# Performance work log

Hardware: AMD Instinct MI355X
Metric: run time of the kernel (lower is better)

Reference implementation:

```python
import jax, jax.numpy as jnp
import numpy as np

N, CM, CZ, COPM = 256, 384, 128, 32
HS, DHS = 8, 48   # row-attention heads / head dim (HS*DHS == CM)
HT, DHT = 4, 32   # triangle-attention heads / head dim


def _param_shapes():
    d = {'opm_ln': (2, CM), 'opm_lr_w': (2, CM, COPM), 'opm_lr_b': (2, COPM),
         'opm_out_w': (COPM, COPM, CZ), 'opm_out_b': (CZ,),
         'ra_ln': (2, CM), 'ra_pair_ln': (2, CZ), 'ra_feat_w': (CZ, HS),
         'ra_qkv_w': (3, CM, HS, DHS), 'ra_gate_w': (CM, HS, DHS), 'ra_gate_b': (HS, DHS),
         'ra_o_w': (HS, DHS, CM), 'ra_o_b': (CM,),
         'st_ln': (2, CM), 'st_w1': (CM, 4 * CM), 'st_b1': (4 * CM,), 'st_w2': (4 * CM, CM), 'st_b2': (CM,)}
    for p in ('tmo', 'tmi'):
        d.update({p + '_ln': (2, CZ), p + '_lr_w': (2, CZ, CZ), p + '_lr_b': (2, CZ),
                  p + '_gate_w': (2, CZ, CZ), p + '_gate_b': (2, CZ), p + '_cln': (2, CZ),
                  p + '_out_w': (CZ, CZ), p + '_out_b': (CZ,), p + '_og_w': (CZ, CZ), p + '_og_b': (CZ,)})
    for p in ('tas', 'tae'):
        d.update({p + '_ln': (2, CZ), p + '_feat_w': (CZ, HT), p + '_qkv_w': (3, CZ, HT, DHT),
                  p + '_gate_w': (CZ, HT, DHT), p + '_gate_b': (HT, DHT),
                  p + '_o_w': (HT, DHT, CZ), p + '_o_b': (CZ,)})
    d.update({'pt_ln': (2, CZ), 'pt_w1': (CZ, 4 * CZ), 'pt_b1': (4 * CZ,),
              'pt_w2': (4 * CZ, CZ), 'pt_b2': (CZ,)})
    return d

_PNAMES = list(_param_shapes().keys())


def setup_inputs():
    keys = iter(jax.random.split(jax.random.key(0), 64))
    inp = {'single_act': jax.random.normal(next(keys), (1, N, CM), jnp.float32),
           'pair_act': jax.random.normal(next(keys), (N, N, CZ), jnp.float32),
           'single_mask': jnp.ones((1, N), jnp.float32),
           'pair_mask': jnp.ones((N, N), jnp.float32)}
    for name, shp in _param_shapes().items():
        p = 0.1 * jax.random.normal(next(keys), shp, jnp.float32)
        if name.endswith('_ln') or name.endswith('_cln'):
            p = p.at[0].add(1.0)  # LayerNorm scale centered at 1
        inp[name] = p
    return inp


def _ln(x, p, eps=1e-5):
    mu = jnp.mean(x, -1, keepdims=True)
    var = jnp.var(x, -1, keepdims=True)
    return (x - mu) * jax.lax.rsqrt(var + eps) * p[0] + p[1]


def _attn(q_data, m_data, bias, nb, qkv_w, gw, gb, ow, ob):
    # AlphaFold gated attention with nonbatched pair bias.
    dh = qkv_w.shape[-1]
    q = jnp.einsum('bqa,ahc->bqhc', q_data, qkv_w[0]) * (dh ** -0.5)
    k = jnp.einsum('bka,ahc->bkhc', m_data, qkv_w[1])
    v = jnp.einsum('bka,ahc->bkhc', m_data, qkv_w[2])
    logits = jnp.einsum('bqhc,bkhc->bhqk', q, k) + bias + nb[None]
    w = jax.nn.softmax(logits, axis=-1)
    wa = jnp.einsum('bhqk,bkhc->bqhc', w, v)
    wa = wa * jax.nn.sigmoid(jnp.einsum('bqc,chv->bqhv', q_data, gw) + gb)
    return jnp.einsum('bqhc,hco->bqo', wa, ow) + ob


def _opm(single, mask1, ln_p, lr_w, lr_b, out_w, out_b):
    # Outer-stack(product)-mean: single [S=1,N,CM] -> pair update [N,N,CZ]
    x = _ln(single, ln_p)
    m = mask1[..., None]
    left = m * (x @ lr_w[0] + lr_b[0])    # [1,N,COPM]
    right = m * (x @ lr_w[1] + lr_b[1])
    act = jnp.einsum('abc,ade->dceb', left, right)          # [N,COPM,COPM,N]
    act = jnp.einsum('dceb,cef->dbf', act, out_w) + out_b   # [N,N,CZ]
    norm = jnp.einsum('abc,adc->bdc', m, m)                 # [N,N,1]
    return act / (1e-3 + norm)


def _tri_mult(pair, mask2, ln_p, lr_w, lr_b, gw, gb, cln, out_w, out_b, og_w, og_b, outgoing):
    m = mask2[..., None]
    x = _ln(pair, ln_p)
    left = m * (x @ lr_w[0] + lr_b[0]) * jax.nn.sigmoid(x @ gw[0] + gb[0])
    right = m * (x @ lr_w[1] + lr_b[1]) * jax.nn.sigmoid(x @ gw[1] + gb[1])
    eq = 'ikc,jkc->ijc' if outgoing else 'kjc,kic->ijc'
    out = jnp.einsum(eq, left, right)
    out = _ln(out, cln) @ out_w + out_b
    out = out * jax.nn.sigmoid(x @ og_w + og_b)
    return pair + out


def _tri_attn(pair, mask2, ln_p, feat_w, qkv_w, gw, gb, ow, ob, per_column):
    pa = jnp.swapaxes(pair, 0, 1) if per_column else pair
    mk = jnp.swapaxes(mask2, 0, 1) if per_column else mask2
    x = _ln(pa, ln_p)
    bias = (1e9 * (mk - 1.0))[:, None, None, :]
    nb = jnp.einsum('qkc,ch->hqk', x, feat_w)
    out = _attn(x, x, bias, nb, qkv_w, gw, gb, ow, ob)
    if per_column:
        out = jnp.swapaxes(out, 0, 1)
    return pair + out


def _fwd(sa, pa, sm, pm, p):
    # 1) outer stack mean -> pair residual
    pa = pa + _opm(sa, sm, p['opm_ln'], p['opm_lr_w'], p['opm_lr_b'], p['opm_out_w'], p['opm_out_b'])
    # 2) row attention with pair bias
    x = _ln(sa, p['ra_ln'])
    bias = (1e9 * (sm - 1.0))[:, None, None, :]
    nb = jnp.einsum('qkc,ch->hqk', _ln(pa, p['ra_pair_ln']), p['ra_feat_w'])
    sa = sa + _attn(x, x, bias, nb, p['ra_qkv_w'], p['ra_gate_w'], p['ra_gate_b'], p['ra_o_w'], p['ra_o_b'])
    # 3) single transition
    x = _ln(sa, p['st_ln'])
    sa = sa + jax.nn.relu(x @ p['st_w1'] + p['st_b1']) @ p['st_w2'] + p['st_b2']
    # 4/5) triangle multiplications
    ko = ('ln', 'lr_w', 'lr_b', 'gate_w', 'gate_b', 'cln', 'out_w', 'out_b', 'og_w', 'og_b')
    pa = _tri_mult(pa, pm, *[p['tmo_' + k] for k in ko], outgoing=True)
    pa = _tri_mult(pa, pm, *[p['tmi_' + k] for k in ko], outgoing=False)
    # 6/7) triangle attentions
    ka = ('ln', 'feat_w', 'qkv_w', 'gate_w', 'gate_b', 'o_w', 'o_b')
    pa = _tri_attn(pa, pm, *[p['tas_' + k] for k in ka], per_column=False)
    pa = _tri_attn(pa, pm, *[p['tae_' + k] for k in ka], per_column=True)
    # 8) pair transition
    x = _ln(pa, p['pt_ln'])
    pa = pa + jax.nn.relu(x @ p['pt_w1'] + p['pt_b1']) @ p['pt_w2'] + p['pt_b2']
    return sa, pa


def reference(single_act, pair_act, single_mask, pair_mask,
              opm_ln, opm_lr_w, opm_lr_b, opm_out_w, opm_out_b,
              ra_ln, ra_pair_ln, ra_feat_w, ra_qkv_w, ra_gate_w, ra_gate_b, ra_o_w, ra_o_b,
              st_ln, st_w1, st_b1, st_w2, st_b2,
              tmo_ln, tmo_lr_w, tmo_lr_b, tmo_gate_w, tmo_gate_b, tmo_cln, tmo_out_w, tmo_out_b, tmo_og_w, tmo_og_b,
              tmi_ln, tmi_lr_w, tmi_lr_b, tmi_gate_w, tmi_gate_b, tmi_cln, tmi_out_w, tmi_out_b, tmi_og_w, tmi_og_b,
              tas_ln, tas_feat_w, tas_qkv_w, tas_gate_w, tas_gate_b, tas_o_w, tas_o_b,
              tae_ln, tae_feat_w, tae_qkv_w, tae_gate_w, tae_gate_b, tae_o_w, tae_o_b,
              pt_ln, pt_w1, pt_b1, pt_w2, pt_b2):
    args = dict(locals())
    p = {k: args[k] for k in _PNAMES}
    return _fwd(single_act, pair_act, single_mask, pair_mask, p)
```

## Files before the change

kernel.cpp:

```cpp
#include <hip/hip_runtime.h>
#include <math.h>

typedef long long i64;
#define NN_ 65536L

typedef __attribute__((ext_vector_type(8))) short bf16x8;
typedef __attribute__((ext_vector_type(4))) float f32x4;

__device__ inline unsigned short f2bf(float f){
  unsigned int u = __float_as_uint(f);
  return (unsigned short)((u + 0x7FFFu + ((u>>16)&1u)) >> 16);
}

__global__ __launch_bounds__(256) void copy_k(float* __restrict__ d, const float* __restrict__ s, long n){
  long i = (long)blockIdx.x*blockDim.x + threadIdx.x;
  if (i < n) d[i] = s[i];
}

__global__ __launch_bounds__(256) void chw2hwc_k(const float* __restrict__ in, float* __restrict__ out){
  __shared__ float t[32][33];
  int r0 = blockIdx.x*32, c0 = blockIdx.y*32;
  int tx = threadIdx.x & 31, ty = threadIdx.x >> 5;
  for (int i = ty; i < 32; i += 8) t[i][tx] = in[(i64)(c0+i)*NN_ + r0 + tx];
  __syncthreads();
  for (int i = ty; i < 32; i += 8) out[(i64)(r0+i)*128 + c0 + tx] = t[tx][i];
}

__global__ __launch_bounds__(256) void tr_mask_k(const float* __restrict__ in, const float* __restrict__ mask,
                                                 float* __restrict__ out){
  __shared__ float t[32][33];
  int r0 = blockIdx.x*32, c0 = blockIdx.y*32;
  int tx = threadIdx.x & 31, ty = threadIdx.x >> 5;
  for (int i = ty; i < 32; i += 8) t[i][tx] = in[(i64)(r0+i)*128 + c0 + tx];
  __syncthreads();
  for (int i = ty; i < 32; i += 8) out[(i64)(c0+i)*NN_ + r0 + tx] = t[tx][i] * mask[r0+tx];
}

__global__ __launch_bounds__(256) void nbQ_k(const float* __restrict__ in, float* __restrict__ out){
  int qq = blockIdx.x, kk = threadIdx.x;
  float4 vv = *(const float4*)(in + ((i64)qq*256 + kk)*4);
  out[0*65536 + qq*256 + kk] = vv.x;
  out[1*65536 + qq*256 + kk] = vv.y;
  out[2*65536 + qq*256 + kk] = vv.z;
  out[3*65536 + qq*256 + kk] = vv.w;
}

__global__ __launch_bounds__(128) void ln_k(const float* __restrict__ in, float* __restrict__ out,
                                            const float* __restrict__ w, int C){
  i64 row = blockIdx.x;
  const float* x = in + row*C;
  float* y = out + row*C;
  int tid = threadIdx.x;
  float s=0.f, s2=0.f;
  for (int c=tid;c<C;c+=128){ float v = x[c]; s += v; s2 += v*v; }
  __shared__ float rs[128], rq[128];
  rs[tid]=s; rq[tid]=s2; __syncthreads();
  for (int off=64;off>0;off>>=1){ if (tid<off){ rs[tid]+=rs[tid+off]; rq[tid]+=rq[tid+off]; } __syncthreads(); }
  float mu = rs[0]/C;
  float var = rq[0]/C - mu*mu;
  float inv = rsqrtf(var + 1e-5f);
  for (int c=tid;c<C;c+=128) y[c] = (x[c]-mu)*inv*w[c] + w[C+c];
}

__global__ __launch_bounds__(256) void ln128_k(const float* __restrict__ in, float* __restrict__ out,
                                               const float* __restrict__ w, int T){
  int wv = threadIdx.x >> 6, lane = threadIdx.x & 63;
  i64 row = (i64)blockIdx.x*4 + wv;
  i64 rr = T ? (i64)((((int)row & 255) << 8) | ((int)row >> 8)) : row;
  float2 v = *(const float2*)(in + rr*128 + lane*2);
  float s = v.x + v.y, s2 = v.x*v.x + v.y*v.y;
  #pragma unroll
  for (int off=32; off; off>>=1){ s += __shfl_down(s, off); s2 += __shfl_down(s2, off); }
  s = __shfl(s, 0); s2 = __shfl(s2, 0);
  float mu = s*(1.f/128.f);
  float var = s2*(1.f/128.f) - mu*mu;
  float inv = rsqrtf(var + 1e-5f);
  float2 wl = *(const float2*)(w + lane*2);
  float2 wb = *(const float2*)(w + 128 + lane*2);
  float2 y; y.x = (v.x-mu)*inv*wl.x + wb.x; y.y = (v.y-mu)*inv*wl.y + wb.y;
  *(float2*)(out + row*128 + lane*2) = y;
}

template<bool TA, bool TB>
__global__ __launch_bounds__(256) void mgemm_k(
    const float* __restrict__ A, int lda, i64 sA,
    const float* __restrict__ B, int ldb, i64 sB,
    float* __restrict__ C, int ldc, i64 sC,
    int M, int N, int K,
    const float* __restrict__ bias, float scale, int act,
    const float* __restrict__ rowmul, int combine, const float* __restrict__ aux)
{
  A += (i64)blockIdx.z * sA;
  B += (i64)blockIdx.z * sB;
  C += (i64)blockIdx.z * sC;
  int m0 = blockIdx.x * 128, n0 = blockIdx.y * 128;
  int tid = threadIdx.x;
  int wave = tid >> 6, lane = tid & 63;
  int quad = lane >> 4, mr = lane & 15;
  int wm = (wave >> 1) * 64, wn = (wave & 1) * 64;
  __shared__ unsigned short As[128][40];
  __shared__ unsigned short Bs[128][40];
  f32x4 acc[4][4];
  #pragma unroll
  for (int i=0;i<4;i++)
    #pragma unroll
    for (int j=0;j<4;j++) acc[i][j] = (f32x4){0.f,0.f,0.f,0.f};

  for (int k0 = 0; k0 < K; k0 += 32){
    if (!TA){
      #pragma unroll
      for (int it=0; it<4; it++){
        int lin = tid + it*256;
        int r = lin >> 3, c4 = (lin & 7) * 4;
        float4 g = *(const float4*)&A[(i64)(m0+r)*lda + k0 + c4];
        As[r][c4]   = f2bf(g.x); As[r][c4+1] = f2bf(g.y);
        As[r][c4+2] = f2bf(g.z); As[r][c4+3] = f2bf(g.w);
      }
    } else {
      #pragma unroll
      for (int it=0; it<4; it++){
        int lin = tid + it*256;
        int m = lin & 127, kg = (lin >> 7) * 4;
        float v0 = A[(i64)(k0+kg  )*lda + m0 + m];
        float v1 = A[(i64)(k0+kg+1)*lda + m0 + m];
        float v2 = A[(i64)(k0+kg+2)*lda + m0 + m];
        float v3 = A[(i64)(k0+kg+3)*lda + m0 + m];
        As[m][kg] = f2bf(v0); As[m][kg+1] = f2bf(v1);
        As[m][kg+2] = f2bf(v2); As[m][kg+3] = f2bf(v3);
      }
    }
    if (!TB){
      #pragma unroll
      for (int it=0; it<4; it++){
        int lin = tid + it*256;
        int n = lin & 127, kg = (lin >> 7) * 4;
        float v0 = B[(i64)(k0+kg  )*ldb + n0 + n];
        float v1 = B[(i64)(k0+kg+1)*ldb + n0 + n];
        float v2 = B[(i64)(k0+kg+2)*ldb + n0 + n];
        float v3 = B[(i64)(k0+kg+3)*ldb + n0 + n];
        Bs[n][kg] = f2bf(v0); Bs[n][kg+1] = f2bf(v1);
        Bs[n][kg+2] = f2bf(v2); Bs[n][kg+3] = f2bf(v3);
      }
    } else {
      #pragma unroll
      for (int it=0; it<4; it++){
        int lin = tid + it*256;
        int r = lin >> 3, c4 = (lin & 7) * 4;
        float4 g = *(const float4*)&B[(i64)(n0+r)*ldb + k0 + c4];
        Bs[r][c4]   = f2bf(g.x); Bs[r][c4+1] = f2bf(g.y);
        Bs[r][c4+2] = f2bf(g.z); Bs[r][c4+3] = f2bf(g.w);
      }
    }
    __syncthreads();
    bf16x8 af[4], bfr[4];
    #pragma unroll
    for (int i=0;i<4;i++) af[i]  = *(const bf16x8*)&As[wm + i*16 + mr][quad*8];
    #pragma unroll
    for (int j=0;j<4;j++) bfr[j] = *(const bf16x8*)&Bs[wn + j*16 + mr][quad*8];
    #pragma unroll
    for (int i=0;i<4;i++)
      #pragma unroll
      for (int j=0;j<4;j++)
        acc[i][j] = __builtin_amdgcn_mfma_f32_16x16x32_bf16(af[i], bfr[j], acc[i][j], 0, 0, 0);
    __syncthreads();
  }
  #pragma unroll
  for (int i=0;i<4;i++){
    #pragma unroll
    for (int r=0;r<4;r++){
      int m = m0 + wm + i*16 + quad*4 + r;
      float rm = rowmul ? rowmul[m] : 1.f;
      i64 mrow = (combine == 4) ? (i64)(((m & 255) << 8) | (m >> 8)) : (i64)m;
      #pragma unroll
      for (int j=0;j<4;j++){
        int n = n0 + wn + j*16 + mr;
        float v = acc[i][j][r] * scale;
        if (bias) v += bias[n];
        if (act == 1) v = fmaxf(v, 0.f);
        else if (act == 2) v = 1.f/(1.f + __expf(-v));
        v *= rm;
        i64 idx = mrow*ldc + n;
        if (combine == 0) C[idx] = v;
        else if (combine == 1 || combine == 4) C[idx] += v;
        else if (combine == 2) C[idx] *= v;
        else C[idx] += aux[(i64)m*ldc + n] * v;
      }
    }
  }
}

template<bool TA, bool TB>
__global__ __launch_bounds__(256) void mgemm64_k(
    const float* __restrict__ A, int lda, i64 sA,
    const float* __restrict__ B, int ldb, i64 sB,
    float* __restrict__ C, int ldc, i64 sC,
    int M, int N, int K,
    const float* __restrict__ bias, float scale, int act,
    const float* __restrict__ rowmul, int combine, const float* __restrict__ aux)
{
  A += (i64)blockIdx.z * sA;
  B += (i64)blockIdx.z * sB;
  C += (i64)blockIdx.z * sC;
  int m0 = blockIdx.x * 64, n0 = blockIdx.y * 64;
  int tid = threadIdx.x;
  int wave = tid >> 6, lane = tid & 63;
  int quad = lane >> 4, mr = lane & 15;
  int wm = (wave >> 1) * 32, wn = (wave & 1) * 32;
  __shared__ unsigned short As[64][40];
  __shared__ unsigned short Bs[64][40];
  f32x4 acc[2][2];
  #pragma unroll
  for (int i=0;i<2;i++)
    #pragma unroll
    for (int j=0;j<2;j++) acc[i][j] = (f32x4){0.f,0.f,0.f,0.f};

  for (int k0 = 0; k0 < K; k0 += 32){
    if (!TA){
      #pragma unroll
      for (int it=0; it<2; it++){
        int lin = tid + it*256;
        int r = lin >> 3, c4 = (lin & 7) * 4;
        float4 g = *(const float4*)&A[(i64)(m0+r)*lda + k0 + c4];
        As[r][c4]   = f2bf(g.x); As[r][c4+1] = f2bf(g.y);
        As[r][c4+2] = f2bf(g.z); As[r][c4+3] = f2bf(g.w);
      }
    } else {
      #pragma unroll
      for (int it=0; it<2; it++){
        int lin = tid + it*256;
        int m = lin & 63, kg = (lin >> 6) * 4;
        float v0 = A[(i64)(k0+kg  )*lda + m0 + m];
        float v1 = A[(i64)(k0+kg+1)*lda + m0 + m];
        float v2 = A[(i64)(k0+kg+2)*lda + m0 + m];
        float v3 = A[(i64)(k0+kg+3)*lda + m0 + m];
        As[m][kg] = f2bf(v0); As[m][kg+1] = f2bf(v1);
        As[m][kg+2] = f2bf(v2); As[m][kg+3] = f2bf(v3);
      }
    }
    if (!TB){
      #pragma unroll
      for (int it=0; it<2; it++){
        int lin = tid + it*256;
        int n = lin & 63, kg = (lin >> 6) * 4;
        float v0 = B[(i64)(k0+kg  )*ldb + n0 + n];
        float v1 = B[(i64)(k0+kg+1)*ldb + n0 + n];
        float v2 = B[(i64)(k0+kg+2)*ldb + n0 + n];
        float v3 = B[(i64)(k0+kg+3)*ldb + n0 + n];
        Bs[n][kg] = f2bf(v0); Bs[n][kg+1] = f2bf(v1);
        Bs[n][kg+2] = f2bf(v2); Bs[n][kg+3] = f2bf(v3);
      }
    } else {
      #pragma unroll
      for (int it=0; it<2; it++){
        int lin = tid + it*256;
        int r = lin >> 3, c4 = (lin & 7) * 4;
        float4 g = *(const float4*)&B[(i64)(n0+r)*ldb + k0 + c4];
        Bs[r][c4]   = f2bf(g.x); Bs[r][c4+1] = f2bf(g.y);
        Bs[r][c4+2] = f2bf(g.z); Bs[r][c4+3] = f2bf(g.w);
      }
    }
    __syncthreads();
    bf16x8 af[2], bfr[2];
    #pragma unroll
    for (int i=0;i<2;i++) af[i]  = *(const bf16x8*)&As[wm + i*16 + mr][quad*8];
    #pragma unroll
    for (int j=0;j<2;j++) bfr[j] = *(const bf16x8*)&Bs[wn + j*16 + mr][quad*8];
    #pragma unroll
    for (int i=0;i<2;i++)
      #pragma unroll
      for (int j=0;j<2;j++)
        acc[i][j] = __builtin_amdgcn_mfma_f32_16x16x32_bf16(af[i], bfr[j], acc[i][j], 0, 0, 0);
    __syncthreads();
  }
  #pragma unroll
  for (int i=0;i<2;i++){
    #pragma unroll
    for (int r=0;r<4;r++){
      int m = m0 + wm + i*16 + quad*4 + r;
      float rm = rowmul ? rowmul[m] : 1.f;
      i64 mrow = (combine == 4) ? (i64)(((m & 255) << 8) | (m >> 8)) : (i64)m;
      #pragma unroll
      for (int j=0;j<2;j++){
        int n = n0 + wn + j*16 + mr;
        float v = acc[i][j][r] * scale;
        if (bias) v += bias[n];
        if (act == 1) v = fmaxf(v, 0.f);
        else if (act == 2) v = 1.f/(1.f + __expf(-v));
        v *= rm;
        i64 idx = mrow*ldc + n;
        if (combine == 0) C[idx] = v;
        else if (combine == 1 || combine == 4) C[idx] += v;
        else if (combine == 2) C[idx] *= v;
        else C[idx] += aux[(i64)m*ldc + n] * v;
      }
    }
  }
}

__global__ __launch_bounds__(256) void mlrgate_k(
    const float* __restrict__ X,
    const float* __restrict__ Wl, const float* __restrict__ bl,
    const float* __restrict__ Wg, const float* __restrict__ bg,
    float* __restrict__ Out)
{
  int m0 = blockIdx.x * 64, n0 = blockIdx.y * 64;
  int tid = threadIdx.x;
  int wave = tid >> 6, lane = tid & 63;
  int quad = lane >> 4, mr = lane & 15;
  int wm = (wave >> 1) * 32, wn = (wave & 1) * 32;
  __shared__ unsigned short As[64][40], B1s[64][40], B2s[64][40];
  f32x4 acc1[2][2], acc2[2][2];
  #pragma unroll
  for (int i=0;i<2;i++)
    #pragma unroll
    for (int j=0;j<2;j++){ acc1[i][j] = (f32x4){0,0,0,0}; acc2[i][j] = (f32x4){0,0,0,0}; }

  for (int k0 = 0; k0 < 128; k0 += 32){
    #pragma unroll
    for (int it=0; it<2; it++){
      int lin = tid + it*256;
      int r = lin >> 3, c4 = (lin & 7) * 4;
      float4 g = *(const float4*)&X[(i64)(m0+r)*128 + k0 + c4];
      As[r][c4]   = f2bf(g.x); As[r][c4+1] = f2bf(g.y);
      As[r][c4+2] = f2bf(g.z); As[r][c4+3] = f2bf(g.w);
    }
    #pragma unroll
    for (int it=0; it<2; it++){
      int lin = tid + it*256;
      int n = lin & 63, kg = (lin >> 6) * 4;
      float a0 = Wl[(i64)(k0+kg  )*128 + n0 + n];
      float a1 = Wl[(i64)(k0+kg+1)*128 + n0 + n];
      float a2 = Wl[(i64)(k0+kg+2)*128 + n0 + n];
      float a3 = Wl[(i64)(k0+kg+3)*128 + n0 + n];
      B1s[n][kg] = f2bf(a0); B1s[n][kg+1] = f2bf(a1);
      B1s[n][kg+2] = f2bf(a2); B1s[n][kg+3] = f2bf(a3);
      float g0 = Wg[(i64)(k0+kg  )*128 + n0 + n];
      float g1 = Wg[(i64)(k0+kg+1)*128 + n0 + n];
      float g2 = Wg[(i64)(k0+kg+2)*128 + n0 + n];
      float g3 = Wg[(i64)(k0+kg+3)*128 + n0 + n];
      B2s[n][kg] = f2bf(g0); B2s[n][kg+1] = f2bf(g1);
      B2s[n][kg+2] = f2bf(g2); B2s[n][kg+3] = f2bf(g3);
    }
    __syncthreads();
    bf16x8 af[2], b1f[2], b2f[2];
    #pragma unroll
    for (int i=0;i<2;i++) af[i]  = *(const bf16x8*)&As[wm + i*16 + mr][quad*8];
    #pragma unroll
    for (int j=0;j<2;j++){
      b1f[j] = *(const bf16x8*)&B1s[wn + j*16 + mr][quad*8];
      b2f[j] = *(const bf16x8*)&B2s[wn + j*16 + mr][quad*8];
    }
    #pragma unroll
    for (int i=0;i<2;i++)
      #pragma unroll
      for (int j=0;j<2;j++){
        acc1[i][j] = __builtin_amdgcn_mfma_f32_16x16x32_bf16(af[i], b1f[j], acc1[i][j], 0, 0, 0);
        acc2[i][j] = __builtin_amdgcn_mfma_f32_16x16x32_bf16(af[i], b2f[j], acc2[i][j], 0, 0, 0);
      }
    __syncthreads();
  }
  #pragma unroll
  for (int i=0;i<2;i++){
    #pragma unroll
    for (int r=0;r<4;r++){
      int m = m0 + wm + i*16 + quad*4 + r;
      #pragma unroll
      for (int j=0;j<2;j++){
        int n = wn + j*16 + mr;
        float lv = acc1[i][j][r] + bl[n0 + n];
        float gv = acc2[i][j][r] + bg[n0 + n];
        Out[(i64)m*128 + n0 + n] = lv * (1.f/(1.f + __expf(-gv)));
      }
    }
  }
}

__global__ __launch_bounds__(256) void ptw1_k(
    const float* __restrict__ X, const float* __restrict__ W1,
    const float* __restrict__ b1, unsigned short* __restrict__ H)
{
  int m0 = blockIdx.x * 128, n0 = blockIdx.y * 128;
  int tid = threadIdx.x;
  int wave = tid >> 6, lane = tid & 63;
  int quad = lane >> 4, mr = lane & 15;
  int wm = (wave >> 1) * 64, wn = (wave & 1) * 64;
  __shared__ unsigned short As[128][40];
  __shared__ unsigned short Bs[128][40];
  f32x4 acc[4][4];
  #pragma unroll
  for (int i=0;i<4;i++)
    #pragma unroll
    for (int j=0;j<4;j++) acc[i][j] = (f32x4){0.f,0.f,0.f,0.f};

  for (int k0 = 0; k0 < 128; k0 += 32){
    #pragma unroll
    for (int it=0; it<4; it++){
      int lin = tid + it*256;
      int r = lin >> 3, c4 = (lin & 7) * 4;
      float4 g = *(const float4*)&X[(i64)(m0+r)*128 + k0 + c4];
      As[r][c4]   = f2bf(g.x); As[r][c4+1] = f2bf(g.y);
      As[r][c4+2] = f2bf(g.z); As[r][c4+3] = f2bf(g.w);
    }
    #pragma unroll
    for (int it=0; it<4; it++){
      int lin = tid + it*256;
      int n = lin & 127, kg = (lin >> 7) * 4;
      float v0 = W1[(i64)(k0+kg  )*512 + n0 + n];
      float v1 = W1[(i64)(k0+kg+1)*512 + n0 + n];
      float v2 = W1[(i64)(k0+kg+2)*512 + n0 + n];
      float v3 = W1[(i64)(k0+kg+3)*512 + n0 + n];
      Bs[n][kg] = f2bf(v0); Bs[n][kg+1] = f2bf(v1);
      Bs[n][kg+2] = f2bf(v2); Bs[n][kg+3] = f2bf(v3);
    }
    __syncthreads();
    bf16x8 af[4], bfr[4];
    #pragma unroll
    for (int i=0;i<4;i++) af[i]  = *(const bf16x8*)&As[wm + i*16 + mr][quad*8];
    #pragma unroll
    for (int j=0;j<4;j++) bfr[j] = *(const bf16x8*)&Bs[wn + j*16 + mr][quad*8];
    #pragma unroll
    for (int i=0;i<4;i++)
      #pragma unroll
      for (int j=0;j<4;j++)
        acc[i][j] = __builtin_amdgcn_mfma_f32_16x16x32_bf16(af[i], bfr[j], acc[i][j], 0, 0, 0);
    __syncthreads();
  }
  #pragma unroll
  for (int i=0;i<4;i++){
    #pragma unroll
    for (int r=0;r<4;r++){
      int m = m0 + wm + i*16 + quad*4 + r;
      #pragma unroll
      for (int j=0;j<4;j++){
        int n = n0 + wn + j*16 + mr;
        float v = fmaxf(acc[i][j][r] + b1[n], 0.f);
        H[(i64)m*512 + n] = f2bf(v);
      }
    }
  }
}

__global__ __launch_bounds__(256) void ptw2_k(
    const unsigned short* __restrict__ H, const float* __restrict__ W2,
    const float* __restrict__ b2, float* __restrict__ pa)
{
  int m0 = blockIdx.x * 64, n0 = blockIdx.y * 64;
  int tid = threadIdx.x;
  int wave = tid >> 6, lane = tid & 63;
  int quad = lane >> 4, mr = lane & 15;
  int wm = (wave >> 1) * 32, wn = (wave & 1) * 32;
  __shared__ unsigned short As[64][40];
  __shared__ unsigned short Bs[64][40];
  f32x4 acc[2][2];
  #pragma unroll
  for (int i=0;i<2;i++)
    #pragma unroll
    for (int j=0;j<2;j++) acc[i][j] = (f32x4){0.f,0.f,0.f,0.f};

  for (int k0 = 0; k0 < 512; k0 += 32){
    #pragma unroll
    for (int it=0; it<2; it++){
      int lin = tid + it*256;
      int r = lin >> 3, c4 = (lin & 7) * 4;
      *(uint2*)&As[r][c4] = *(const uint2*)&H[(i64)(m0+r)*512 + k0 + c4];
    }
    #pragma unroll
    for (int it=0; it<2; it++){
      int lin = tid + it*256;
      int n = lin & 63, kg = (lin >> 6) * 4;
      float v0 = W2[(i64)(k0+kg  )*128 + n0 + n];
      float v1 = W2[(i64)(k0+kg+1)*128 + n0 + n];
      float v2 = W2[(i64)(k0+kg+2)*128 + n0 + n];
      float v3 = W2[(i64)(k0+kg+3)*128 + n0 + n];
      Bs[n][kg] = f2bf(v0); Bs[n][kg+1] = f2bf(v1);
      Bs[n][kg+2] = f2bf(v2); Bs[n][kg+3] = f2bf(v3);
    }
    __syncthreads();
    bf16x8 af[2], bfr[2];
    #pragma unroll
    for (int i=0;i<2;i++) af[i]  = *(const bf16x8*)&As[wm + i*16 + mr][quad*8];
    #pragma unroll
    for (int j=0;j<2;j++) bfr[j] = *(const bf16x8*)&Bs[wn + j*16 + mr][quad*8];
    #pragma unroll
    for (int i=0;i<2;i++)
      #pragma unroll
      for (int j=0;j<2;j++)
        acc[i][j] = __builtin_amdgcn_mfma_f32_16x16x32_bf16(af[i], bfr[j], acc[i][j], 0, 0, 0);
    __syncthreads();
  }
  #pragma unroll
  for (int i=0;i<2;i++){
    #pragma unroll
    for (int r=0;r<4;r++){
      int m = m0 + wm + i*16 + quad*4 + r;
      #pragma unroll
      for (int j=0;j<2;j++){
        int n = n0 + wn + j*16 + mr;
        pa[(i64)m*128 + n] += acc[i][j][r] + b2[n];
      }
    }
  }
}

template<bool TA, bool TB>
__global__ __launch_bounds__(256) void gemm_k(
    const float* __restrict__ A, int lda, i64 sA,
    const float* __restrict__ B, int ldb, i64 sB,
    float* __restrict__ C, int ldc, i64 sC,
    int M, int N, int K,
    const float* __restrict__ bias, float scale, int act,
    const float* __restrict__ rowmul, int combine)
{
  A += (i64)blockIdx.z * sA;
  B += (i64)blockIdx.z * sB;
  C += (i64)blockIdx.z * sC;
  int m0 = blockIdx.x * 64, n0 = blockIdx.y * 64;
  int tid = threadIdx.x, tx = tid & 15, ty = tid >> 4;
  __shared__ float As[16][68], Bs[16][68];
  float acc[4][4] = {};
  for (int k0 = 0; k0 < K; k0 += 16){
    if (TA){
      for (int l = tid; l < 1024; l += 256){
        int kk = l >> 6, mi = l & 63; int m = m0 + mi;
        As[kk][mi] = (m < M) ? A[(i64)(k0+kk)*lda + m] : 0.f;
      }
    } else {
      for (int l = tid; l < 1024; l += 256){
        int mi = l >> 4, kk = l & 15; int m = m0 + mi;
        As[kk][mi] = (m < M) ? A[(i64)m*lda + k0 + kk] : 0.f;
      }
    }
    if (TB){
      for (int l = tid; l < 1024; l += 256){
        int ni = l >> 4, kk = l & 15; int n = n0 + ni;
        Bs[kk][ni] = (n < N) ? B[(i64)n*ldb + k0 + kk] : 0.f;
      }
    } else {
      for (int l = tid; l < 1024; l += 256){
        int kk = l >> 6, ni = l & 63; int n = n0 + ni;
        Bs[kk][ni] = (n < N) ? B[(i64)(k0+kk)*ldb + n] : 0.f;
      }
    }
    __syncthreads();
    #pragma unroll
    for (int kk = 0; kk < 16; ++kk){
      float4 av4 = *(const float4*)&As[kk][ty*4];
      float4 bv4 = *(const float4*)&Bs[kk][tx*4];
      float av[4] = {av4.x, av4.y, av4.z, av4.w};
      float bv[4] = {bv4.x, bv4.y, bv4.z, bv4.w};
      #pragma unroll
      for (int i=0;i<4;i++)
        #pragma unroll
        for (int j=0;j<4;j++) acc[i][j] = fmaf(av[i], bv[j], acc[i][j]);
    }
    __syncthreads();
  }
  #pragma unroll
  for (int i=0;i<4;i++){
    int m = m0 + ty*4 + i;
    if (m >= M) continue;
    float rm = rowmul ? rowmul[m] : 1.f;
    #pragma unroll
    for (int j=0;j<4;j++){
      int n = n0 + tx*4 + j;
      if (n >= N) continue;
      float v = acc[i][j] * scale;
      if (bias) v += bias[n];
      if (act == 1) v = fmaxf(v, 0.f);
      else if (act == 2) v = 1.f/(1.f + expf(-v));
      v *= rm;
      i64 idx = (i64)m*ldc + n;
      if (combine == 0) C[idx] = v;
      else if (combine == 1) C[idx] += v;
      else C[idx] *= v;
    }
  }
}

__global__ __launch_bounds__(256) void gemm_part_k(
    const float* __restrict__ A, int lda,
    const float* __restrict__ B, int ldb,
    float* __restrict__ Cp, int M, int N, int K, int chunk)
{
  int m0 = blockIdx.x*16, n0 = blockIdx.y*64, z = blockIdx.z;
  int kb = z*chunk, ke = min(K, kb+chunk);
  int tid = threadIdx.x;
  int mi = tid >> 4, ni4 = (tid & 15)*4;
  __shared__ float As[16][17], Bs[16][68];
  float acc[4] = {0.f,0.f,0.f,0.f};
  for (int k0 = kb; k0 < ke; k0 += 16){
    { int r = tid>>4, c = tid&15; int m = m0+r;
      As[c][r] = (m < M) ? A[(i64)m*lda + k0 + c] : 0.f; }
    for (int l = tid; l < 1024; l += 256){
      int kk = l>>6, nn = l&63; int n = n0+nn;
      Bs[kk][nn] = (n < N) ? B[(i64)(k0+kk)*ldb + n] : 0.f;
    }
    __syncthreads();
    #pragma unroll
    for (int kk=0;kk<16;kk++){
      float a = As[kk][mi];
      float4 b = *(const float4*)&Bs[kk][ni4];
      acc[0]=fmaf(a,b.x,acc[0]); acc[1]=fmaf(a,b.y,acc[1]);
      acc[2]=fmaf(a,b.z,acc[2]); acc[3]=fmaf(a,b.w,acc[3]);
    }
    __syncthreads();
  }
  int m = m0+mi, n = n0+ni4;
  if (m < M && n < N) *(float4*)&Cp[((i64)z*M + m)*N + n] = *(float4*)acc;
}

__global__ __launch_bounds__(256) void gemm_reduce_k(
    const float* __restrict__ Cp, float* __restrict__ C, int ldc,
    int M, int N, int S,
    const float* __restrict__ bias, float scale, int act,
    const float* __restrict__ rowmul, int combine)
{
  i64 idx = (i64)blockIdx.x*256 + threadIdx.x;
  if (idx >= (i64)M*N) return;
  int m = (int)(idx / N), n = (int)(idx % N);
  float s = 0.f;
  for (int z=0; z<S; z++) s += Cp[(i64)z*M*N + idx];
  float v = s*scale;
  if (bias) v += bias[n];
  if (act == 1) v = fmaxf(v, 0.f);
  else if (act == 2) v = 1.f/(1.f + expf(-v));
  if (rowmul) v *= rowmul[m];
  i64 o = (i64)m*ldc + n;
  if (combine == 0) C[o] = v;
  else if (combine == 1) C[o] += v;
  else C[o] *= v;
}

__global__ __launch_bounds__(128) void opm_wd_k(const float* __restrict__ right, const float* __restrict__ W,
                                                float* __restrict__ Wd){
  int d = blockIdx.x, c = blockIdx.y, f = threadIdx.x;
  float acc = 0.f;
  #pragma unroll
  for (int e=0;e<32;e++) acc = fmaf(right[d*32+e], W[((i64)c*32+e)*128 + f], acc);
  Wd[((i64)d*32+c)*128 + f] = acc;
}

__global__ __launch_bounds__(128) void opm_final_k(const float* __restrict__ left, const float* __restrict__ Wd,
                                                   const float* __restrict__ ob, const float* __restrict__ sm,
                                                   const float* __restrict__ pair_act, float* __restrict__ pa){
  int d = blockIdx.x, b0 = blockIdx.y*16, f = threadIdx.x;
  __shared__ float wd_s[32][128];
  __shared__ float l_s[16][32];
  for (int c=0;c<32;c++) wd_s[c][f] = Wd[((i64)d*32+c)*128 + f];
  for (int l = f; l < 512; l += 128){ int bi=l>>5, c=l&31; l_s[bi][c] = left[(b0+bi)*32 + c]; }
  __syncthreads();
  float md = sm[d], obf = ob[f];
  for (int bi=0;bi<16;bi++){
    float acc = 0.f;
    #pragma unroll
    for (int c=0;c<32;c++) acc = fmaf(l_s[bi][c], wd_s[c][f], acc);
    int b = b0+bi;
    i64 idx = ((i64)d*256 + b)*128 + f;
    pa[idx] = pair_act[idx] + (acc + obf) / (1e-3f + md*sm[b]);
  }
}

__global__ __launch_bounds__(256) void ra_attn_k(const float* __restrict__ q, const float* __restrict__ k,
                                                 const float* __restrict__ v, const float* __restrict__ nb,
                                                 const float* __restrict__ sm, float* __restrict__ wa){
  int qi = blockIdx.x, h = blockIdx.y, tid = threadIdx.x;
  __shared__ float qv[48];
  __shared__ float p[256];
  __shared__ float red[256];
  if (tid < 48) qv[tid] = q[(i64)qi*384 + h*48 + tid];
  __syncthreads();
  float acc = 0.f;
  const float* kr = k + (i64)tid*384 + h*48;
  #pragma unroll
  for (int c=0;c<48;c++) acc = fmaf(qv[c], kr[c], acc);
  acc += 1e9f*(sm[tid]-1.f) + nb[((i64)qi*256 + tid)*8 + h];
  red[tid] = acc; __syncthreads();
  for (int off=128;off>0;off>>=1){ if (tid<off) red[tid] = fmaxf(red[tid], red[tid+off]); __syncthreads(); }
  float mx = red[0]; __syncthreads();
  float e = expf(acc - mx);
  red[tid] = e; __syncthreads();
  for (int off=128;off>0;off>>=1){ if (tid<off) red[tid] += red[tid+off]; __syncthreads(); }
  p[tid] = e / red[0];
  __syncthreads();
  if (tid < 48){
    float a = 0.f;
    for (int kk=0;kk<256;kk++) a = fmaf(p[kk], v[(i64)kk*384 + h*48 + tid], a);
    wa[(i64)qi*384 + h*48 + tid] = a;
  }
}

__global__ __launch_bounds__(256, 6) void ta_mfma_k(
    const float* __restrict__ q, const float* __restrict__ k, const float* __restrict__ v,
    const float* __restrict__ nbQ, const float* __restrict__ mask, int maskT,
    float* __restrict__ wa)
{
  int qblk = blockIdx.x, h = blockIdx.y, b = blockIdx.z;
  int tid = threadIdx.x;
  int wave = tid >> 6, lane = tid & 63;
  int quad = lane >> 4, mr = lane & 15;
  const i64 base = ((i64)b*256)*128 + h*32;

  __shared__ __align__(16) unsigned short Ks[128][40];
  __shared__ __align__(16) unsigned short Vt[32][136];
  __shared__ __align__(16) float mask_s[256];
  __shared__ __align__(16) unsigned short Pl[4][16][40];

  mask_s[tid] = 1e9f * ((maskT ? mask[(i64)tid*256 + b] : mask[(i64)b*256 + tid]) - 1.f);

  int q0w = qblk*64 + wave*16;
  int qg = q0w + mr;
  const float* nbq = nbQ + (i64)h*65536 + (i64)qg*256;

  bf16x8 qf;
  {
    const float* qp = q + base + (i64)qg*128 + quad*8;
    float4 a = *(const float4*)qp;
    float4 c = *(const float4*)(qp+4);
    qf[0]=(short)f2bf(a.x); qf[1]=(short)f2bf(a.y); qf[2]=(short)f2bf(a.z); qf[3]=(short)f2bf(a.w);
    qf[4]=(short)f2bf(c.x); qf[5]=(short)f2bf(c.y); qf[6]=(short)f2bf(c.z); qf[7]=(short)f2bf(c.w);
  }

  f32x4 o0 = (f32x4){0,0,0,0}, o1 = (f32x4){0,0,0,0};
  float mm = -1e30f, ll = 0.f;

  for (int half = 0; half < 2; half++){
    __syncthreads();
    #pragma unroll
    for (int it=0; it<4; it++){
      int idx = it*256 + tid;
      int kl = idx >> 3, c4 = (idx & 7)*4;
      i64 roff = base + (i64)(half*128 + kl)*128 + c4;
      float4 g  = *(const float4*)(k + roff);
      unsigned int w0 = (unsigned int)f2bf(g.x) | ((unsigned int)f2bf(g.y)<<16);
      unsigned int w1 = (unsigned int)f2bf(g.z) | ((unsigned int)f2bf(g.w)<<16);
      *(uint2*)&Ks[kl][c4] = make_uint2(w0, w1);
      float4 gv = *(const float4*)(v + roff);
      Vt[c4  ][kl] = f2bf(gv.x);
      Vt[c4+1][kl] = f2bf(gv.y);
      Vt[c4+2][kl] = f2bf(gv.z);
      Vt[c4+3][kl] = f2bf(gv.w);
    }
    __syncthreads();

    #pragma unroll
    for (int it=0; it<4; it++){
      int kc = it*32;
      int kg = half*128 + kc;
      bf16x8 kf0 = *(const bf16x8*)&Ks[kc + mr][quad*8];
      bf16x8 kf1 = *(const bf16x8*)&Ks[kc + 16 + mr][quad*8];
      f32x4 s0 = __builtin_amdgcn_mfma_f32_16x16x32_bf16(kf0, qf, (f32x4){0,0,0,0}, 0, 0, 0);
      f32x4 s1 = __builtin_amdgcn_mfma_f32_16x16x32_bf16(kf1, qf, (f32x4){0,0,0,0}, 0, 0, 0);
      float4 nb0 = *(const float4*)(nbq + kg + quad*4);
      float4 nb1 = *(const float4*)(nbq + kg + 16 + quad*4);
      float4 mk0 = *(const float4*)&mask_s[kg + quad*4];
      float4 mk1 = *(const float4*)&mask_s[kg + 16 + quad*4];
      s0[0] += nb0.x + mk0.x; s0[1] += nb0.y + mk0.y; s0[2] += nb0.z + mk0.z; s0[3] += nb0.w + mk0.w;
      s1[0] += nb1.x + mk1.x; s1[1] += nb1.y + mk1.y; s1[2] += nb1.z + mk1.z; s1[3] += nb1.w + mk1.w;

      float tm = fmaxf(fmaxf(fmaxf(s0[0],s0[1]), fmaxf(s0[2],s0[3])),
                       fmaxf(fmaxf(s1[0],s1[1]), fmaxf(s1[2],s1[3])));
      tm = fmaxf(tm, __shfl_xor(tm, 16));
      tm = fmaxf(tm, __shfl_xor(tm, 32));
      float nm = fmaxf(mm, tm);
      float alpha = __expf(mm - nm);
      mm = nm;
      float e00 = __expf(s0[0]-nm), e01 = __expf(s0[1]-nm);
      float e02 = __expf(s0[2]-nm), e03 = __expf(s0[3]-nm);
      float e10 = __expf(s1[0]-nm), e11 = __expf(s1[1]-nm);
      float e12 = __expf(s1[2]-nm), e13 = __expf(s1[3]-nm);
      float ps = ((e00+e01) + (e02+e03)) + ((e10+e11) + (e12+e13));
      ps += __shfl_xor(ps, 16);
      ps += __shfl_xor(ps, 32);
      ll = ll*alpha + ps;
      o0 *= alpha; o1 *= alpha;
      unsigned int p0 = (unsigned int)f2bf(e00) | ((unsigned int)f2bf(e01)<<16);
      unsigned int p1 = (unsigned int)f2bf(e02) | ((unsigned int)f2bf(e03)<<16);
      unsigned int p2 = (unsigned int)f2bf(e10) | ((unsigned int)f2bf(e11)<<16);
      unsigned int p3 = (unsigned int)f2bf(e12) | ((unsigned int)f2bf(e13)<<16);
      *(uint2*)&Pl[wave][mr][quad*4]      = make_uint2(p0, p1);
      *(uint2*)&Pl[wave][mr][16 + quad*4] = make_uint2(p2, p3);
      bf16x8 pf  = *(const bf16x8*)&Pl[wave][mr][quad*8];
      bf16x8 vf0 = *(const bf16x8*)&Vt[mr     ][kc + quad*8];
      bf16x8 vf1 = *(const bf16x8*)&Vt[16 + mr][kc + quad*8];
      o0 = __builtin_amdgcn_mfma_f32_16x16x32_bf16(vf0, pf, o0, 0, 0, 0);
      o1 = __builtin_amdgcn_mfma_f32_16x16x32_bf16(vf1, pf, o1, 0, 0, 0);
    }
  }

  float inv = 1.f/ll;
  float* wp = wa + base + (i64)qg*128;
  *(float4*)(wp + quad*4)      = make_float4(o0[0]*inv, o0[1]*inv, o0[2]*inv, o0[3]*inv);
  *(float4*)(wp + 16 + quad*4) = make_float4(o1[0]*inv, o1[1]*inv, o1[2]*inv, o1[3]*inv);
}

static void gemm(hipStream_t st, bool TA, bool TB,
                 const float* A, int lda, i64 sA,
                 const float* B, int ldb, i64 sB,
                 float* C, int ldc, i64 sC,
                 int M, int N, int K, int batch,
                 const float* bias, float scale, int act,
                 const float* rowmul, int combine)
{
  dim3 g((M+63)/64, (N+63)/64, batch), bl(256);
  if (!TA && !TB)      gemm_k<false,false><<<g,bl,0,st>>>(A,lda,sA,B,ldb,sB,C,ldc,sC,M,N,K,bias,scale,act,rowmul,combine);
  else if (!TA &&  TB) gemm_k<false,true ><<<g,bl,0,st>>>(A,lda,sA,B,ldb,sB,C,ldc,sC,M,N,K,bias,scale,act,rowmul,combine);
  else                 gemm_k<true ,false><<<g,bl,0,st>>>(A,lda,sA,B,ldb,sB,C,ldc,sC,M,N,K,bias,scale,act,rowmul,combine);
}

static void mgemm(hipStream_t st, bool TA, bool TB,
                  const float* A, int lda, i64 sA,
                  const float* B, int ldb, i64 sB,
                  float* C, int ldc, i64 sC,
                  int M, int N, int K, int batch,
                  const float* bias, float scale, int act,
                  const float* rowmul, int combine, const float* aux = nullptr)
{
  dim3 bl(256);
  i64 nb128 = (i64)(M/128)*(N/128)*batch;
  if (nb128 < 1024 && (M % 64) == 0 && (N % 64) == 0){
    dim3 g(M/64, N/64, batch);
    if (!TA && !TB)      mgemm64_k<false,false><<<g,bl,0,st>>>(A,lda,sA,B,ldb,sB,C,ldc,sC,M,N,K,bias,scale,act,rowmul,combine,aux);
    else if (!TA &&  TB) mgemm64_k<false,true ><<<g,bl,0,st>>>(A,lda,sA,B,ldb,sB,C,ldc,sC,M,N,K,bias,scale,act,rowmul,combine,aux);
    else                 mgemm64_k<true ,false><<<g,bl,0,st>>>(A,lda,sA,B,ldb,sB,C,ldc,sC,M,N,K,bias,scale,act,rowmul,combine,aux);
    return;
  }
  dim3 g(M/128, N/128, batch);
  if (!TA && !TB)      mgemm_k<false,false><<<g,bl,0,st>>>(A,lda,sA,B,ldb,sB,C,ldc,sC,M,N,K,bias,scale,act,rowmul,combine,aux);
  else if (!TA &&  TB) mgemm_k<false,true ><<<g,bl,0,st>>>(A,lda,sA,B,ldb,sB,C,ldc,sC,M,N,K,bias,scale,act,rowmul,combine,aux);
  else                 mgemm_k<true ,false><<<g,bl,0,st>>>(A,lda,sA,B,ldb,sB,C,ldc,sC,M,N,K,bias,scale,act,rowmul,combine,aux);
}

static void gemm_thin(hipStream_t st,
                      const float* A, int lda, const float* B, int ldb,
                      float* C, int ldc, int M, int N, int K,
                      const float* bias, float scale, int act,
                      const float* rowmul, int combine, float* part)
{
  const int S = 8;
  int chunk = ((K/S + 15)/16)*16; if (chunk < 16) chunk = 16;
  dim3 g((M+15)/16, (N+63)/64, S);
  gemm_part_k<<<g,256,0,st>>>(A,lda,B,ldb,part,M,N,K,chunk);
  i64 t = (i64)M*N;
  gemm_reduce_k<<<(int)((t+255)/256),256,0,st>>>(part,C,ldc,M,N,S,bias,scale,act,rowmul,combine);
}

extern "C" void kernel_launch(void* const* d_in, const int* in_sizes, int n_in,
                              void* d_out, int out_size, void* d_ws, size_t ws_size,
                              hipStream_t stream)
{
  const float* IN[64];
  for (int i=0;i<n_in && i<64;i++) IN[i] = (const float*)d_in[i];

  const float* single_act = IN[0];
  const float* pair_act   = IN[1];
  const float* sm         = IN[2];
  const float* pm         = IN[3];
  const float* opm_ln     = IN[4];
  const float* opm_lr_w   = IN[5];
  const float* opm_lr_b   = IN[6];
  const float* opm_out_w  = IN[7];
  const float* opm_out_b  = IN[8];
  const float* ra_ln      = IN[9];
  const float* ra_pair_ln = IN[10];
  const float* ra_feat_w  = IN[11];
  const float* ra_qkv_w   = IN[12];
  const float* ra_gate_w  = IN[13];
  const float* ra_gate_b  = IN[14];
  const float* ra_o_w     = IN[15];
  const float* ra_o_b     = IN[16];
  const float* st_ln      = IN[17];
  const float* st_w1      = IN[18];
  const float* st_b1      = IN[19];
  const float* st_w2      = IN[20];
  const float* st_b2      = IN[21];
  const float* pt_ln      = IN[56];
  const float* pt_w1      = IN[57];
  const float* pt_b1      = IN[58];
  const float* pt_w2      = IN[59];
  const float* pt_b2      = IN[60];

  float* sa = (float*)d_out;
  float* pa = (float*)d_out + 98304;

  float* W  = (float*)d_ws;
  float* B0 = W;
  float* B1 = W + 8388608L;
  float* B2 = W + 16777216L;
  float* B3 = W + 25165824L;
  float* SMA = W + 33554432L;
  float* xs   = SMA;
  float* qb   = SMA +  98304;
  float* kb   = SMA + 196608;
  float* vb   = SMA + 294912;
  float* wab  = SMA + 393216;
  float* hst  = SMA + 491520;
  float* nbra = SMA + 884736;
  float* lbuf = SMA + 1409024;
  float* rbuf = SMA + 1417216;
  float* Wd   = SMA + 1425408;
  float* nbt  = SMA + 2473984;

  copy_k<<<384, 256, 0, stream>>>(sa, single_act, 98304L);

  ln_k<<<256,128,0,stream>>>(single_act, xs, opm_ln, 384);
  gemm_thin(stream, xs,384, opm_lr_w,32,       lbuf,32, 256,32,384, opm_lr_b,    1.f,0, sm,0, B1);
  gemm_thin(stream, xs,384, opm_lr_w+12288,32, rbuf,32, 256,32,384, opm_lr_b+32, 1.f,0, sm,0, B1);
  opm_wd_k<<<dim3(256,32),128,0,stream>>>(rbuf, opm_out_w, Wd);
  opm_final_k<<<dim3(256,16),128,0,stream>>>(lbuf, Wd, opm_out_b, sm, pair_act, pa);

  ln_k<<<256,128,0,stream>>>(sa, xs, ra_ln, 384);
  ln128_k<<<16384,256,0,stream>>>(pa, B0, ra_pair_ln, 0);
  gemm(stream,false,false, B0,128,0, ra_feat_w,8,0, nbra,8,0, 65536,8,128,1, nullptr,1.f,0,nullptr,0);
  const float qs_ra = 0.14433756729740643f;
  gemm_thin(stream, xs,384, ra_qkv_w,384,        qb,384, 256,384,384, nullptr,qs_ra,0,nullptr,0, B1);
  gemm_thin(stream, xs,384, ra_qkv_w+147456,384, kb,384, 256,384,384, nullptr,1.f,0,nullptr,0, B1);
  gemm_thin(stream, xs,384, ra_qkv_w+294912,384, vb,384, 256,384,384, nullptr,1.f,0,nullptr,0, B1);
  ra_attn_k<<<dim3(256,8),256,0,stream>>>(qb, kb, vb, nbra, sm, wab);
  gemm_thin(stream, xs,384,  ra_gate_w,384, wab,384, 256,384,384, ra_gate_b,1.f,2,nullptr,2, B1);
  gemm_thin(stream, wab,384, ra_o_w,384,    sa,384,  256,384,384, ra_o_b,   1.f,0,nullptr,1, B1);

  ln_k<<<256,128,0,stream>>>(sa, xs, st_ln, 384);
  gemm_thin(stream, xs,384,   st_w1,1536, hst,1536, 256,1536,384, st_b1,1.f,1,nullptr,0, B1);
  gemm_thin(stream, hst,1536, st_w2,384,  sa,384,   256,384,1536, st_b2,1.f,0,nullptr,1, B1);

  auto tri_mult = [&](int base, bool outgoing){
    const float* ln_w = IN[base+0];
    const float* lr_w = IN[base+1];
    const float* lr_b = IN[base+2];
    const float* gw   = IN[base+3];
    const float* gb   = IN[base+4];
    const float* cln  = IN[base+5];
    const float* ow   = IN[base+6];
    const float* ob   = IN[base+7];
    const float* ogw  = IN[base+8];
    const float* ogb  = IN[base+9];
    ln128_k<<<16384,256,0,stream>>>(pa, B0, ln_w, 0);
    mlrgate_k<<<dim3(1024,2),256,0,stream>>>(B0, lr_w, lr_b, gw, gb, B3);
    tr_mask_k<<<dim3(2048,4),256,0,stream>>>(B3, pm, B1);
    mlrgate_k<<<dim3(1024,2),256,0,stream>>>(B0, lr_w+16384, lr_b+128, gw+16384, gb+128, B3);
    tr_mask_k<<<dim3(2048,4),256,0,stream>>>(B3, pm, B2);
    if (outgoing)
      mgemm(stream,false,true, B1,256,65536, B2,256,65536, B3,256,65536, 256,256,256,128, nullptr,1.f,0,nullptr,0);
    else
      mgemm(stream,true,false, B2,256,65536, B1,256,65536, B3,256,65536, 256,256,256,128, nullptr,1.f,0,nullptr,0);
    chw2hwc_k<<<dim3(2048,4),256,0,stream>>>(B3, B1);
    ln128_k<<<16384,256,0,stream>>>(B1, B3, cln, 0);
    mgemm(stream,false,false, B3,128,0, ow,128,0,  B1,128,0, 65536,128,128,1, ob,  1.f,0,nullptr,0);
    mgemm(stream,false,false, B0,128,0, ogw,128,0, pa,128,0, 65536,128,128,1, ogb, 1.f,2,nullptr,3, B1);
  };
  tri_mult(22, true);
  tri_mult(32, false);

  auto tri_attn = [&](int base, bool percol){
    const float* ln_w   = IN[base+0];
    const float* feat_w = IN[base+1];
    const float* qkv_w  = IN[base+2];
    const float* gw     = IN[base+3];
    const float* gb     = IN[base+4];
    const float* ow     = IN[base+5];
    const float* ob     = IN[base+6];
    ln128_k<<<16384,256,0,stream>>>(pa, B0, ln_w, percol?1:0);
    gemm(stream,false,false, B0,128,0, feat_w,4,0, nbt,4,0, 65536,4,128,1, nullptr,1.f,0,nullptr,0);
    nbQ_k<<<256,256,0,stream>>>(nbt, nbra);
    const float qs = 0.17677669529663687f;
    mgemm(stream,false,false, B0,128,0, qkv_w,128,0,       B1,128,0, 65536,128,128,1, nullptr,qs, 0,nullptr,0);
    mgemm(stream,false,false, B0,128,0, qkv_w+16384,128,0, B2,128,0, 65536,128,128,1, nullptr,1.f,0,nullptr,0);
    mgemm(stream,false,false, B0,128,0, qkv_w+32768,128,0, B3,128,0, 65536,128,128,1, nullptr,1.f,0,nullptr,0);
    ta_mfma_k<<<dim3(4,4,256),256,0,stream>>>(B1, B2, B3, nbra, pm, percol?1:0, B1);
    mgemm(stream,false,false, B0,128,0, gw,128,0, B1,128,0, 65536,128,128,1, gb,1.f,2,nullptr,2);
    mgemm(stream,false,false, B1,128,0, ow,128,0, pa,128,0, 65536,128,128,1, ob,1.f,0,nullptr, percol?4:1);
  };
  tri_attn(42, false);
  tri_attn(49, true);

  ln128_k<<<16384,256,0,stream>>>(pa, B0, pt_ln, 0);
  ptw1_k<<<dim3(512,4),256,0,stream>>>(B0, pt_w1, pt_b1, (unsigned short*)B1);
  ptw2_k<<<dim3(1024,2),256,0,stream>>>((const unsigned short*)B1, pt_w2, pt_b2, pa);
}
```

Before: 1.465 ms.

## Replace narrow feature GEMMs with dedicated kernels and remap triangle-attention blocks per XCD

The generic GEMM for the 4- and 8-wide bias feature projections is replaced by dedicated per-row dot-product kernels. The 4-head variant writes directly in head-major layout, which removes the separate nbQ transpose kernel and its temporary buffer. The triangle-attention grid is flattened to 1D and remapped so each XCD handles a contiguous range of batch rows. This is meant to improve L2 locality of the K/V reads shared across heads and query blocks. The new kernels use scalar FMAs, and each thread reads a full 512-byte row, so loads are strided across lanes.

```diff
diff --git a/kernel.cpp b/kernel.cpp
--- a/kernel.cpp
+++ b/kernel.cpp
@@ -36,13 +36,49 @@
   for (int i = ty; i < 32; i += 8) out[(i64)(c0+i)*NN_ + r0 + tx] = t[tx][i] * mask[r0+tx];
 }
 
-__global__ __launch_bounds__(256) void nbQ_k(const float* __restrict__ in, float* __restrict__ out){
-  int qq = blockIdx.x, kk = threadIdx.x;
-  float4 vv = *(const float4*)(in + ((i64)qq*256 + kk)*4);
-  out[0*65536 + qq*256 + kk] = vv.x;
-  out[1*65536 + qq*256 + kk] = vv.y;
-  out[2*65536 + qq*256 + kk] = vv.z;
-  out[3*65536 + qq*256 + kk] = vv.w;
+__global__ __launch_bounds__(256) void feat4_k(const float* __restrict__ X, const float* __restrict__ W,
+                                               float* __restrict__ out){
+  __shared__ float4 w_s[128];
+  int q = blockIdx.x, k = threadIdx.x;
+  if (k < 128) w_s[k] = *(const float4*)(W + k*4);
+  __syncthreads();
+  const float* x = X + ((i64)q*256 + k)*128;
+  float a0=0.f, a1=0.f, a2=0.f, a3=0.f;
+  #pragma unroll
+  for (int c=0;c<128;c+=4){
+    float4 v = *(const float4*)(x+c);
+    float4 w0 = w_s[c], w1 = w_s[c+1], w2 = w_s[c+2], w3 = w_s[c+3];
+    a0 = fmaf(v.x,w0.x,a0); a1 = fmaf(v.x,w0.y,a1); a2 = fmaf(v.x,w0.z,a2); a3 = fmaf(v.x,w0.w,a3);
+    a0 = fmaf(v.y,w1.x,a0); a1 = fmaf(v.y,w1.y,a1); a2 = fmaf(v.y,w1.z,a2); a3 = fmaf(v.y,w1.w,a3);
+    a0 = fmaf(v.z,w2.x,a0); a1 = fmaf(v.z,w2.y,a1); a2 = fmaf(v.z,w2.z,a2); a3 = fmaf(v.z,w2.w,a3);
+    a0 = fmaf(v.w,w3.x,a0); a1 = fmaf(v.w,w3.y,a1); a2 = fmaf(v.w,w3.z,a2); a3 = fmaf(v.w,w3.w,a3);
+  }
+  i64 o = (i64)q*256 + k;
+  out[o] = a0; out[65536+o] = a1; out[131072+o] = a2; out[196608+o] = a3;
+}
+
+__global__ __launch_bounds__(256) void feat8_k(const float* __restrict__ X, const float* __restrict__ W,
+                                               float* __restrict__ out){
+  __shared__ float w_s[128][8];
+  int q = blockIdx.x, k = threadIdx.x;
+  for (int i = k; i < 1024; i += 256) ((float*)w_s)[i] = W[i];
+  __syncthreads();
+  const float* x = X + ((i64)q*256 + k)*128;
+  float acc[8] = {};
+  #pragma unroll
+  for (int c=0;c<128;c+=4){
+    float4 v = *(const float4*)(x+c);
+    #pragma unroll
+    for (int h=0;h<8;h++){
+      acc[h] = fmaf(v.x, w_s[c  ][h], acc[h]);
+      acc[h] = fmaf(v.y, w_s[c+1][h], acc[h]);
+      acc[h] = fmaf(v.z, w_s[c+2][h], acc[h]);
+      acc[h] = fmaf(v.w, w_s[c+3][h], acc[h]);
+    }
+  }
+  float* o = out + ((i64)q*256 + k)*8;
+  *(float4*)o     = make_float4(acc[0],acc[1],acc[2],acc[3]);
+  *(float4*)(o+4) = make_float4(acc[4],acc[5],acc[6],acc[7]);
 }
 
 __global__ __launch_bounds__(128) void ln_k(const float* __restrict__ in, float* __restrict__ out,
@@ -694,7 +730,11 @@
     const float* __restrict__ nbQ, const float* __restrict__ mask, int maskT,
     float* __restrict__ wa)
 {
-  int qblk = blockIdx.x, h = blockIdx.y, b = blockIdx.z;
+  int d = blockIdx.x;
+  int xcd = d & 7, y = d >> 3;
+  int b = xcd*32 + (y >> 4);
+  int w = y & 15;
+  int qblk = w & 3, h = w >> 2;
   int tid = threadIdx.x;
   int wave = tid >> 6, lane = tid & 63;
   int quad = lane >> 4, mr = lane & 15;
@@ -898,7 +938,6 @@
   float* lbuf = SMA + 1409024;
   float* rbuf = SMA + 1417216;
   float* Wd   = SMA + 1425408;
-  float* nbt  = SMA + 2473984;
 
   copy_k<<<384, 256, 0, stream>>>(sa, single_act, 98304L);
 
@@ -910,7 +949,7 @@
 
   ln_k<<<256,128,0,stream>>>(sa, xs, ra_ln, 384);
   ln128_k<<<16384,256,0,stream>>>(pa, B0, ra_pair_ln, 0);
-  gemm(stream,false,false, B0,128,0, ra_feat_w,8,0, nbra,8,0, 65536,8,128,1, nullptr,1.f,0,nullptr,0);
+  feat8_k<<<256,256,0,stream>>>(B0, ra_feat_w, nbra);
   const float qs_ra = 0.14433756729740643f;
   gemm_thin(stream, xs,384, ra_qkv_w,384,        qb,384, 256,384,384, nullptr,qs_ra,0,nullptr,0, B1);
   gemm_thin(stream, xs,384, ra_qkv_w+147456,384, kb,384, 256,384,384, nullptr,1.f,0,nullptr,0, B1);
@@ -960,13 +999,12 @@
     const float* ow     = IN[base+5];
     const float* ob     = IN[base+6];
     ln128_k<<<16384,256,0,stream>>>(pa, B0, ln_w, percol?1:0);
-    gemm(stream,false,false, B0,128,0, feat_w,4,0, nbt,4,0, 65536,4,128,1, nullptr,1.f,0,nullptr,0);
-    nbQ_k<<<256,256,0,stream>>>(nbt, nbra);
+    feat4_k<<<256,256,0,stream>>>(B0, feat_w, nbra);
     const float qs = 0.17677669529663687f;
     mgemm(stream,false,false, B0,128,0, qkv_w,128,0,       B1,128,0, 65536,128,128,1, nullptr,qs, 0,nullptr,0);
     mgemm(stream,false,false, B0,128,0, qkv_w+16384,128,0, B2,128,0, 65536,128,128,1, nullptr,1.f,0,nullptr,0);
     mgemm(stream,false,false, B0,128,0, qkv_w+32768,128,0, B3,128,0, 65536,128,128,1, nullptr,1.f,0,nullptr,0);
-    ta_mfma_k<<<dim3(4,4,256),256,0,stream>>>(B1, B2, B3, nbra, pm, percol?1:0, B1);
+    ta_mfma_k<<<dim3(4096),256,0,stream>>>(B1, B2, B3, nbra, pm, percol?1:0, B1);
     mgemm(stream,false,false, B0,128,0, gw,128,0, B1,128,0, 65536,128,128,1, gb,1.f,2,nullptr,2);
     mgemm(stream,false,false, B1,128,0, ow,128,0, pa,128,0, 65536,128,128,1, ob,1.f,0,nullptr, percol?4:1);
   };
```

Result: faster. 1.386 ms (-5.3%).
